# Performance work log

Hardware: AMD Instinct MI355X
Metric: run time of the kernel (lower is better)

Reference implementation:

```python
import jax, jax.numpy as jnp
import numpy as np


def _cross_head_proj(x, sw, qw1, qw2, kw1, kw2, qdd, kdd):
    # x: [B,N,T,S] attention logits/probs; sw: [N,N]
    # qw1/qw2: [B,T,I,N], kw1/kw2: [B,S,I,N] (I=2 dynamic rank), qdd: [B,T,N], kdd: [B,S,N]
    out = x + jnp.einsum('bnts,nm->bmts', x, sw)
    # low-rank dynamic mixing along query positions (sum over i reproduces the range(2) loop)
    qh = jnp.einsum('bnts,btin->bits', x, qw1)          # [B,I,T,S]
    out = out + jnp.einsum('bits,btin->bnts', qh, qw2)
    # low-rank dynamic mixing along key positions
    kh = jnp.einsum('bnts,bsin->bits', x, kw1)          # [B,I,T,S]
    out = out + jnp.einsum('bits,bsin->bnts', kh, kw2)
    # diagonal (per-head) dynamic terms
    out = out + x * jnp.transpose(qdd, (0, 2, 1))[:, :, :, None]   # [B,N,T,1]
    out = out + x * jnp.transpose(kdd, (0, 2, 1))[:, :, None, :]   # [B,N,1,S]
    return out


def setup_inputs() -> dict:
    key = jax.random.key(0)
    ks = jax.random.split(key, 18)
    B, N, T, S, D, I = 1, 32, 1024, 1024, 128, 2
    scale = 0.05  # dynamic weights come out of tanh/RMSnorm in the original; keep them small
    query = jax.random.normal(ks[0], (B, N, T, D), jnp.float32) * (D ** -0.5)
    k_ = jax.random.normal(ks[1], (B, N, S, D), jnp.float32)
    v_ = jax.random.normal(ks[2], (B, N, S, D), jnp.float32)
    neg = jnp.finfo(jnp.float32).min * 0.5  # matches make_causal_mask
    atten_mask = jnp.where(jnp.arange(S)[None, :] <= jnp.arange(T)[:, None], 0.0, neg).astype(jnp.float32)
    def dws(i0):
        return (
            jax.random.normal(ks[i0 + 0], (N, N), jnp.float32) * scale,
            jax.random.normal(ks[i0 + 1], (B, T, I, N), jnp.float32) * scale,
            jax.random.normal(ks[i0 + 2], (B, T, I, N), jnp.float32) * scale,
            jax.random.normal(ks[i0 + 3], (B, S, I, N), jnp.float32) * scale,
            jax.random.normal(ks[i0 + 4], (B, S, I, N), jnp.float32) * scale,
            jax.random.normal(ks[i0 + 5], (B, T, N), jnp.float32) * scale,
            jax.random.normal(ks[i0 + 6], (B, S, N), jnp.float32) * scale,
        )
    sw_pre, qw1_pre, qw2_pre, kw1_pre, kw2_pre, qdd_pre, kdd_pre = dws(3)
    sw_post, qw1_post, qw2_post, kw1_post, kw2_post, qdd_post, kdd_post = dws(10)
    return {
        'query': query, 'key': k_, 'value': v_, 'atten_mask': atten_mask,
        'sw_pre': sw_pre, 'qw1_pre': qw1_pre, 'qw2_pre': qw2_pre, 'kw1_pre': kw1_pre,
        'kw2_pre': kw2_pre, 'qdd_pre': qdd_pre, 'kdd_pre': kdd_pre,
        'sw_post': sw_post, 'qw1_post': qw1_post, 'qw2_post': qw2_post, 'kw1_post': kw1_post,
        'kw2_post': kw2_post, 'qdd_post': qdd_post, 'kdd_post': kdd_post,
    }


def reference(query, key, value, atten_mask,
              sw_pre, qw1_pre, qw2_pre, kw1_pre, kw2_pre, qdd_pre, kdd_pre,
              sw_post, qw1_post, qw2_post, kw1_post, kw2_post, qdd_post, kdd_post):
    # _atten_context: QK^T -> pre cross-head proj -> mask -> softmax -> post cross-head proj -> AV
    logits = jnp.einsum('bntd,bnsd->bnts', query, key)
    logits = _cross_head_proj(logits, sw_pre, qw1_pre, qw2_pre, kw1_pre, kw2_pre, qdd_pre, kdd_pre)
    logits = logits + atten_mask  # [T,S] broadcasts over [B,N,T,S]
    probs = jax.nn.softmax(logits, axis=-1)
    probs = _cross_head_proj(probs, sw_post, qw1_post, qw2_post, kw1_post, kw2_post, qdd_post, kdd_post)
    return jnp.einsum('bnts,bnsd->bntd', probs, value)
```

## Files before the change

kernel.cpp:

```cpp
#include <hip/hip_runtime.h>
#include <hip/hip_bf16.h>
#include <cstdint>
#include <cstddef>

#define T_DIM 1024
#define S_DIM 1024
#define N_HEADS 32
#define D_HEAD 128

typedef __attribute__((ext_vector_type(8))) short short8;
typedef __attribute__((ext_vector_type(4))) float floatx4;

__device__ inline int pack_bf16(float a, float b) {
    __hip_bfloat162 h = __float22bfloat162_rn(make_float2(a, b));
    int r; __builtin_memcpy(&r, &h, 4); return r;
}
__device__ inline ushort f2b(float x) {
    __hip_bfloat16 h = __float2bfloat16(x);
    ushort u; __builtin_memcpy(&u, &h, 2); return u;
}
__device__ inline float b2f(ushort u) {
    unsigned int v = ((unsigned int)u) << 16;
    float f; __builtin_memcpy(&f, &v, 4); return f;
}

__global__ __launch_bounds__(256) void vt_kernel(const float* __restrict__ V,
                                                 ushort* __restrict__ Vt) {
    const int s0 = blockIdx.x * 64;
    const int n  = blockIdx.y;
    __shared__ float lds[128 * 65];

    const int tid = threadIdx.x;
    const float* Vn = V + ((size_t)n * S_DIM + s0) * D_HEAD;

    #pragma unroll
    for (int it = 0; it < 8; ++it) {
        int idx = tid + it * 256;
        int d4 = idx & 31, s = idx >> 5;
        float4 v = *(const float4*)(Vn + (size_t)s * D_HEAD + d4 * 4);
        lds[(d4 * 4 + 0) * 65 + s] = v.x;
        lds[(d4 * 4 + 1) * 65 + s] = v.y;
        lds[(d4 * 4 + 2) * 65 + s] = v.z;
        lds[(d4 * 4 + 3) * 65 + s] = v.w;
    }
    __syncthreads();

    ushort* Vtn = Vt + (size_t)n * D_HEAD * S_DIM;
    #pragma unroll
    for (int it = 0; it < 4; ++it) {
        int idx = tid + it * 256;
        int sg = idx & 7, d = idx >> 3;
        const float* src = &lds[d * 65 + sg * 8];
        int4 o;
        o.x = pack_bf16(src[0], src[1]);
        o.y = pack_bf16(src[2], src[3]);
        o.z = pack_bf16(src[4], src[5]);
        o.w = pack_bf16(src[6], src[7]);
        *(int4*)&Vtn[(size_t)d * S_DIM + s0 + sg * 8] = o;
    }
}

__global__ __launch_bounds__(256, 2) void qk_mfma(const float* __restrict__ Q,
                                                  const float* __restrict__ K,
                                                  ushort* __restrict__ Lb) {
    const int st = blockIdx.x;
    const int tt = blockIdx.y;
    const int n  = blockIdx.z;
    if (st > tt) return;

    __shared__ int Qt[64 * 64];
    __shared__ int Kt[64 * 64];

    const int tid = threadIdx.x;
    const int wv = tid >> 6, ln = tid & 63;
    const int frow = ln & 15, quad = ln >> 4;

    const float* Qn = Q + ((size_t)n * T_DIM + (size_t)tt * 64) * D_HEAD;
    const float* Kn = K + ((size_t)n * S_DIM + (size_t)st * 64) * D_HEAD;

    #pragma unroll
    for (int rep = 0; rep < 8; ++rep) {
        int idx = tid + rep * 256;
        int row = idx >> 5;
        int c4  = (idx & 31) * 4;
        int p   = c4 >> 1;
        int kb  = p >> 4, w = p & 15;
        int swz = 4 * (row & 3);
        float4 q = *(const float4*)(Qn + (size_t)row * D_HEAD + c4);
        int2 qv; qv.x = pack_bf16(q.x, q.y); qv.y = pack_bf16(q.z, q.w);
        *(int2*)&Qt[row * 64 + kb * 16 + (w ^ swz)] = qv;
        float4 k = *(const float4*)(Kn + (size_t)row * D_HEAD + c4);
        int2 kv; kv.x = pack_bf16(k.x, k.y); kv.y = pack_bf16(k.z, k.w);
        *(int2*)&Kt[row * 64 + kb * 16 + (w ^ swz)] = kv;
    }
    __syncthreads();

    const int swz = 4 * (frow & 3);
    floatx4 acc[4] = {};
    #pragma unroll
    for (int kb = 0; kb < 4; ++kb) {
        const short8 af = *(const short8*)&Qt[(wv * 16 + frow) * 64 + kb * 16 + ((quad * 4) ^ swz)];
        #pragma unroll
        for (int si = 0; si < 4; ++si) {
            const short8 bf = *(const short8*)&Kt[(si * 16 + frow) * 64 + kb * 16 + ((quad * 4) ^ swz)];
            acc[si] = __builtin_amdgcn_mfma_f32_16x16x32_bf16(af, bf, acc[si], 0, 0, 0);
        }
    }
    __syncthreads();

    ushort* Ot = (ushort*)Qt;
    #pragma unroll
    for (int si = 0; si < 4; ++si)
        #pragma unroll
        for (int r = 0; r < 4; ++r)
            Ot[(wv * 16 + quad * 4 + r) * 72 + si * 16 + frow] = f2b(acc[si][r]);
    __syncthreads();

    #pragma unroll
    for (int it = 0; it < 2; ++it) {
        int idx = tid + it * 256;
        int row = idx >> 3, col = idx & 7;
        int4 v = *(const int4*)&Ot[row * 72 + col * 8];
        *(int4*)&Lb[((size_t)n * T_DIM + tt * 64 + row) * S_DIM + st * 64 + col * 8] = v;
    }
}

__global__ __launch_bounds__(256) void mat4_kernel(
        const float* __restrict__ sw_pre,  const float* __restrict__ qw1_pre,
        const float* __restrict__ qw2_pre, const float* __restrict__ qdd_pre,
        const float* __restrict__ kw1_pre, const float* __restrict__ kw2_pre,
        const float* __restrict__ kdd_pre,
        const float* __restrict__ sw_post,  const float* __restrict__ qw1_post,
        const float* __restrict__ qw2_post, const float* __restrict__ qdd_post,
        const float* __restrict__ kw1_post, const float* __restrict__ kw2_post,
        const float* __restrict__ kdd_post,
        ushort* __restrict__ mats) {
    const float *sw, *w1, *w2, *dd;
    float idadd;
    switch (blockIdx.y) {
        case 0:  sw = sw_pre;  w1 = qw1_pre;  w2 = qw2_pre;  dd = qdd_pre;  idadd = 1.0f; break;
        case 1:  sw = nullptr; w1 = kw1_pre;  w2 = kw2_pre;  dd = kdd_pre;  idadd = 0.0f; break;
        case 2:  sw = sw_post; w1 = qw1_post; w2 = qw2_post; dd = qdd_post; idadd = 1.0f; break;
        default: sw = nullptr; w1 = kw1_post; w2 = kw2_post; dd = kdd_post; idadd = 0.0f; break;
    }
    ushort* out = mats + (size_t)blockIdx.y * 1024 * 1024;

    const int t = blockIdx.x;
    const int tid = threadIdx.x;
    const int m = tid >> 3;
    const int n0 = (tid & 7) * 4;

    const float w2m0 = w2[t * 64 + m];
    const float w2m1 = w2[t * 64 + 32 + m];
    const float ddm  = dd[t * 32 + m];

    float v[4];
    #pragma unroll
    for (int j = 0; j < 4; ++j) {
        int n = n0 + j;
        float r = w1[t * 64 + n] * w2m0 + w1[t * 64 + 32 + n] * w2m1;
        if (sw) r += sw[n * 32 + m];
        if (n == m) r += idadd + ddm;
        v[j] = r;
    }
    int p0 = pack_bf16(v[0], v[1]);
    int p1 = pack_bf16(v[2], v[3]);
    int2 st = make_int2(p0, p1);
    *(int2*)&out[(size_t)t * 1024 + m * 32 + n0] = st;
}

__global__ __launch_bounds__(256) void rowstat(const ushort* __restrict__ Lb,
                                               float2* __restrict__ stats) {
    const int wv = threadIdx.x >> 6;
    const int ln = threadIdx.x & 63;
    const int r0 = blockIdx.x * 4 + wv;
    const int t  = r0 & (T_DIM - 1);
    const ushort* row = Lb + (size_t)r0 * S_DIM;

    float v[2][8];
    #pragma unroll
    for (int it = 0; it < 2; ++it) {
        const int i0 = it * 512 + ln * 8;
        #pragma unroll
        for (int j = 0; j < 8; ++j) v[it][j] = -INFINITY;
        if (i0 <= t) {
            uint4 raw = *(const uint4*)&row[i0];
            v[it][0] = b2f((ushort)(raw.x & 0xffff)); v[it][1] = b2f((ushort)(raw.x >> 16));
            v[it][2] = b2f((ushort)(raw.y & 0xffff)); v[it][3] = b2f((ushort)(raw.y >> 16));
            v[it][4] = b2f((ushort)(raw.z & 0xffff)); v[it][5] = b2f((ushort)(raw.z >> 16));
            v[it][6] = b2f((ushort)(raw.w & 0xffff)); v[it][7] = b2f((ushort)(raw.w >> 16));
            #pragma unroll
            for (int j = 0; j < 8; ++j)
                if (i0 + j > t) v[it][j] = -INFINITY;
        }
    }

    float m = -INFINITY;
    #pragma unroll
    for (int it = 0; it < 2; ++it)
        #pragma unroll
        for (int j = 0; j < 8; ++j) m = fmaxf(m, v[it][j]);
    #pragma unroll
    for (int off = 32; off > 0; off >>= 1) m = fmaxf(m, __shfl_xor(m, off));

    float ssum = 0.0f;
    #pragma unroll
    for (int it = 0; it < 2; ++it)
        #pragma unroll
        for (int j = 0; j < 8; ++j)
            ssum += (v[it][j] > -1e37f) ? __expf(v[it][j] - m) : 0.0f;
    #pragma unroll
    for (int off = 32; off > 0; off >>= 1) ssum += __shfl_xor(ssum, off);

    if (ln == 0) stats[r0] = make_float2(m, 1.0f / ssum);
}

template<bool SM>
__global__ __launch_bounds__(256, 2) void proj2t(ushort* __restrict__ Lb,
                                                 const ushort* __restrict__ Cmat,
                                                 const ushort* __restrict__ Kmat,
                                                 const float2* __restrict__ stats) {
    const int s0 = blockIdx.x * 32;
    const int t0 = blockIdx.y * 16;
    if (s0 > t0 + 15) return;

    __shared__ __align__(16) ushort Xs[16 * 1288];
    __shared__ __align__(16) float  Kp[16 * 516];

    const int tid = threadIdx.x;
    const int wv = tid >> 6, ln = tid & 63;
    const int frow = ln & 15, quad = ln >> 4;

    #pragma unroll
    for (int it = 0; it < 8; ++it) {
        int slot = tid + it * 256;
        int c    = slot & 3;
        int row  = slot >> 2;
        int nn   = row >> 4, tl = row & 15;
        uint4 ld = *(const uint4*)(Lb + ((size_t)nn * T_DIM + t0 + tl) * S_DIM + s0 + c * 8);
        ushort u[8];
        u[0] = (ushort)(ld.x & 0xffff);  u[1] = (ushort)(ld.x >> 16);
        u[2] = (ushort)(ld.y & 0xffff);  u[3] = (ushort)(ld.y >> 16);
        u[4] = (ushort)(ld.z & 0xffff);  u[5] = (ushort)(ld.z >> 16);
        u[6] = (ushort)(ld.w & 0xffff);  u[7] = (ushort)(ld.w >> 16);
        if (SM) {
            const float2 ms = stats[nn * T_DIM + t0 + tl];
            const int tG = t0 + tl, sbase = s0 + c * 8;
            #pragma unroll
            for (int j = 0; j < 8; ++j) {
                float x = (sbase + j <= tG) ? __expf(b2f(u[j]) - ms.x) * ms.y : 0.0f;
                u[j] = f2b(x);
            }
        }
        ushort* xp = &Xs[tl * 1288 + (c * 8) * 40 + nn];
        #pragma unroll
        for (int j = 0; j < 8; ++j) xp[j * 40] = u[j];
    }
    __syncthreads();

    #pragma unroll
    for (int mh = 0; mh < 2; ++mh) {
        #pragma unroll
        for (int k = 0; k < 8; ++k) {
            const int sl = wv * 8 + k;
            const short8 af = *(const short8*)(Kmat + (size_t)(s0 + sl) * 1024 + (mh * 16 + frow) * 32 + quad * 8);
            const short8 bf = *(const short8*)&Xs[frow * 1288 + sl * 40 + quad * 8];
            floatx4 z = {0.f, 0.f, 0.f, 0.f};
            floatx4 d = __builtin_amdgcn_mfma_f32_16x16x32_bf16(af, bf, z, 0, 0, 0);
            *(floatx4*)&Kp[frow * 516 + sl * 16 + quad * 4] = d;
        }
        __syncthreads();

        #pragma unroll
        for (int i = 0; i < 4; ++i) {
            const int tl = wv * 4 + i;
            const int tg = t0 + tl;
            const short8 bf = *(const short8*)(Cmat + (size_t)tg * 1024 + (mh * 16 + frow) * 32 + quad * 8);
            #pragma unroll
            for (int st = 0; st < 2; ++st) {
                const short8 af = *(const short8*)&Xs[tl * 1288 + (st * 16 + frow) * 40 + quad * 8];
                floatx4 z = {0.f, 0.f, 0.f, 0.f};
                floatx4 d = __builtin_amdgcn_mfma_f32_16x16x32_bf16(af, bf, z, 0, 0, 0);
                float v[4];
                #pragma unroll
                for (int r = 0; r < 4; ++r) {
                    const int sl = st * 16 + quad * 4 + r;
                    float val = d[r] + Kp[tl * 516 + sl * 16 + frow];
                    v[r] = (s0 + sl > tg) ? 0.0f : val;
                }
                uint2 stv;
                stv.x = (unsigned)pack_bf16(v[0], v[1]);
                stv.y = (unsigned)pack_bf16(v[2], v[3]);
                *(uint2*)&Lb[((size_t)(mh * 16 + frow) * T_DIM + tg) * S_DIM + s0 + st * 16 + quad * 4] = stv;
            }
        }
        __syncthreads();
    }
}

__global__ __launch_bounds__(256, 4) void av3(const ushort* __restrict__ P,
                                              const ushort* __restrict__ Vt,
                                              float* __restrict__ O) {
    const int tid = threadIdx.x;
    const int wv = tid >> 6, ln = tid & 63;
    const int frow = ln & 15, quad = ln >> 4;
    const int n  = blockIdx.x;
    const int tt = 63 - blockIdx.y;
    const int t0 = tt * 16;

    __shared__ ushort red[4][16][136];

    const ushort* Pn  = P  + ((size_t)n * T_DIM + t0) * S_DIM;
    const ushort* Vtn = Vt + (size_t)n * D_HEAD * S_DIM;

    const int nsteps = (t0 + 47) >> 5;
    const int nclean = t0 >> 5;

    floatx4 acc[8] = {};
    for (int sb = wv; sb < nsteps; sb += 4) {
        short8 a = *(const short8*)(Pn + (size_t)frow * S_DIM + sb * 32 + quad * 8);
        if (sb >= nclean) {
            const int tg  = t0 + frow;
            const int sg0 = sb * 32 + quad * 8;
            #pragma unroll
            for (int j = 0; j < 8; ++j)
                if (sg0 + j > tg) a[j] = 0;
        }
        #pragma unroll
        for (int dc = 0; dc < 8; ++dc) {
            const short8 b = *(const short8*)(Vtn + (size_t)(dc * 16 + frow) * S_DIM + sb * 32 + quad * 8);
            acc[dc] = __builtin_amdgcn_mfma_f32_16x16x32_bf16(a, b, acc[dc], 0, 0, 0);
        }
    }

    #pragma unroll
    for (int dc = 0; dc < 8; ++dc)
        #pragma unroll
        for (int r = 0; r < 4; ++r)
            red[wv][quad * 4 + r][dc * 16 + frow] = f2b(acc[dc][r]);
    __syncthreads();

    #pragma unroll
    for (int it = 0; it < 2; ++it) {
        int idx = tid + it * 256;
        int d4 = idx & 31, tr = idx >> 5;
        float4 v;
        v.x = b2f(red[0][tr][d4 * 4 + 0]) + b2f(red[1][tr][d4 * 4 + 0]) + b2f(red[2][tr][d4 * 4 + 0]) + b2f(red[3][tr][d4 * 4 + 0]);
        v.y = b2f(red[0][tr][d4 * 4 + 1]) + b2f(red[1][tr][d4 * 4 + 1]) + b2f(red[2][tr][d4 * 4 + 1]) + b2f(red[3][tr][d4 * 4 + 1]);
        v.z = b2f(red[0][tr][d4 * 4 + 2]) + b2f(red[1][tr][d4 * 4 + 2]) + b2f(red[2][tr][d4 * 4 + 2]) + b2f(red[3][tr][d4 * 4 + 2]);
        v.w = b2f(red[0][tr][d4 * 4 + 3]) + b2f(red[1][tr][d4 * 4 + 3]) + b2f(red[2][tr][d4 * 4 + 3]) + b2f(red[3][tr][d4 * 4 + 3]);
        *(float4*)&O[((size_t)n * T_DIM + t0 + tr) * D_HEAD + d4 * 4] = v;
    }
}

extern "C" void kernel_launch(void* const* d_in, const int* in_sizes, int n_in,
                              void* d_out, int out_size, void* d_ws, size_t ws_size,
                              hipStream_t stream) {
    const float* Q    = (const float*)d_in[0];
    const float* K    = (const float*)d_in[1];
    const float* V    = (const float*)d_in[2];
    const float* sw_pre  = (const float*)d_in[4];
    const float* qw1_pre = (const float*)d_in[5];
    const float* qw2_pre = (const float*)d_in[6];
    const float* kw1_pre = (const float*)d_in[7];
    const float* kw2_pre = (const float*)d_in[8];
    const float* qdd_pre = (const float*)d_in[9];
    const float* kdd_pre = (const float*)d_in[10];
    const float* sw_post  = (const float*)d_in[11];
    const float* qw1_post = (const float*)d_in[12];
    const float* qw2_post = (const float*)d_in[13];
    const float* kw1_post = (const float*)d_in[14];
    const float* kw2_post = (const float*)d_in[15];
    const float* qdd_post = (const float*)d_in[16];
    const float* kdd_post = (const float*)d_in[17];

    ushort* Lb = (ushort*)d_ws;
    ushort* Vt = (ushort*)((char*)d_ws + (size_t)N_HEADS * T_DIM * S_DIM * 2);
    float*  O  = (float*)d_out;

    ushort* mats  = (ushort*)d_out;
    ushort* Cpre  = mats + 0 * 1024 * 1024;
    ushort* Kpre  = mats + 1 * 1024 * 1024;
    ushort* Cpost = mats + 2 * 1024 * 1024;
    ushort* Kpost = mats + 3 * 1024 * 1024;
    float2* stats = (float2*)((char*)d_out + (size_t)8 * 1024 * 1024);

    mat4_kernel<<<dim3(1024, 4), 256, 0, stream>>>(
        sw_pre, qw1_pre, qw2_pre, qdd_pre, kw1_pre, kw2_pre, kdd_pre,
        sw_post, qw1_post, qw2_post, qdd_post, kw1_post, kw2_post, kdd_post, mats);
    vt_kernel<<<dim3(16, 32), 256, 0, stream>>>(V, Vt);

    qk_mfma<<<dim3(16, 16, 32), 256, 0, stream>>>(Q, K, Lb);
    proj2t<false><<<dim3(32, 64), 256, 0, stream>>>(Lb, Cpre, Kpre, nullptr);
    rowstat<<<dim3(8192), 256, 0, stream>>>(Lb, stats);
    proj2t<true><<<dim3(32, 64), 256, 0, stream>>>(Lb, Cpost, Kpost, stats);
    av3<<<dim3(32, 64), 256, 0, stream>>>(Lb, Vt, O);
}
```

Measured before the change: 294.1 us.

## Shrink projection kernel LDS with bf16 partials and swizzled head-packed staging

The cross-head projection kernel now stages the logits tile in LDS with a compact XOR-swizzled layout. Each thread loads 8 heads and writes packed 16-byte vectors instead of scattered 2-byte stores. The key-side partial products are kept in LDS as bf16 instead of fp32. Together these cut shared memory so three blocks per CU can fit instead of two, and they reduce LDS store instructions and bank conflicts. The cost is an extra bf16 rounding of the key-mixing partial sum and higher register use for the 8-wide loads.

```diff
diff --git a/kernel.cpp b/kernel.cpp
--- a/kernel.cpp
+++ b/kernel.cpp
@@ -22,6 +22,10 @@
 __device__ inline float b2f(ushort u) {
     unsigned int v = ((unsigned int)u) << 16;
     float f; __builtin_memcpy(&f, &v, 4); return f;
+}
+__device__ inline uint ext16(const uint4& u, int sp) {
+    const uint* p = (const uint*)&u;
+    return (p[sp >> 1] >> ((sp & 1) * 16)) & 0xffffu;
 }
 
 __global__ __launch_bounds__(256) void vt_kernel(const float* __restrict__ V,
@@ -216,45 +220,56 @@
 }
 
 template<bool SM>
-__global__ __launch_bounds__(256, 2) void proj2t(ushort* __restrict__ Lb,
-                                                 const ushort* __restrict__ Cmat,
-                                                 const ushort* __restrict__ Kmat,
-                                                 const float2* __restrict__ stats) {
+__global__ __launch_bounds__(256, 3) void proj3(ushort* __restrict__ Lb,
+                                                const ushort* __restrict__ Cmat,
+                                                const ushort* __restrict__ Kmat,
+                                                const float2* __restrict__ stats) {
     const int s0 = blockIdx.x * 32;
     const int t0 = blockIdx.y * 16;
     if (s0 > t0 + 15) return;
 
-    __shared__ __align__(16) ushort Xs[16 * 1288];
-    __shared__ __align__(16) float  Kp[16 * 516];
+    __shared__ __align__(16) ushort Xs[16 * 1040];
+    __shared__ __align__(16) ushort Kpb[16 * 648];
 
     const int tid = threadIdx.x;
     const int wv = tid >> 6, ln = tid & 63;
     const int frow = ln & 15, quad = ln >> 4;
 
-    #pragma unroll
-    for (int it = 0; it < 8; ++it) {
-        int slot = tid + it * 256;
-        int c    = slot & 3;
-        int row  = slot >> 2;
-        int nn   = row >> 4, tl = row & 15;
-        uint4 ld = *(const uint4*)(Lb + ((size_t)nn * T_DIM + t0 + tl) * S_DIM + s0 + c * 8);
-        ushort u[8];
-        u[0] = (ushort)(ld.x & 0xffff);  u[1] = (ushort)(ld.x >> 16);
-        u[2] = (ushort)(ld.y & 0xffff);  u[3] = (ushort)(ld.y >> 16);
-        u[4] = (ushort)(ld.z & 0xffff);  u[5] = (ushort)(ld.z >> 16);
-        u[6] = (ushort)(ld.w & 0xffff);  u[7] = (ushort)(ld.w >> 16);
+    {
+        const int sc = tid & 3;
+        const int mc = (tid >> 2) & 3;
+        const int tl = tid >> 4;
+        uint4 U[8];
+        #pragma unroll
+        for (int j = 0; j < 8; ++j) {
+            const int n = mc * 8 + j;
+            U[j] = *(const uint4*)(Lb + ((size_t)n * T_DIM + t0 + tl) * S_DIM + s0 + sc * 8);
+        }
         if (SM) {
-            const float2 ms = stats[nn * T_DIM + t0 + tl];
-            const int tG = t0 + tl, sbase = s0 + c * 8;
+            const int tG = t0 + tl;
             #pragma unroll
             for (int j = 0; j < 8; ++j) {
-                float x = (sbase + j <= tG) ? __expf(b2f(u[j]) - ms.x) * ms.y : 0.0f;
-                u[j] = f2b(x);
+                const float2 ms = stats[(mc * 8 + j) * T_DIM + tG];
+                uint* up = (uint*)&U[j];
+                #pragma unroll
+                for (int w = 0; w < 4; ++w) {
+                    const int sg = s0 + sc * 8 + 2 * w;
+                    float lo = (sg     <= tG) ? __expf(b2f((ushort)(up[w] & 0xffff)) - ms.x) * ms.y : 0.0f;
+                    float hi = (sg + 1 <= tG) ? __expf(b2f((ushort)(up[w] >> 16   )) - ms.x) * ms.y : 0.0f;
+                    up[w] = (unsigned)pack_bf16(lo, hi);
+                }
             }
         }
-        ushort* xp = &Xs[tl * 1288 + (c * 8) * 40 + nn];
-        #pragma unroll
-        for (int j = 0; j < 8; ++j) xp[j * 40] = u[j];
+        #pragma unroll
+        for (int sp = 0; sp < 8; ++sp) {
+            const int s = sc * 8 + sp;
+            uint4 W;
+            W.x = ext16(U[0], sp) | (ext16(U[1], sp) << 16);
+            W.y = ext16(U[2], sp) | (ext16(U[3], sp) << 16);
+            W.z = ext16(U[4], sp) | (ext16(U[5], sp) << 16);
+            W.w = ext16(U[6], sp) | (ext16(U[7], sp) << 16);
+            *(uint4*)&Xs[tl * 1040 + s * 32 + ((mc ^ (s & 3)) << 3)] = W;
+        }
     }
     __syncthreads();
 
@@ -264,10 +279,13 @@
         for (int k = 0; k < 8; ++k) {
             const int sl = wv * 8 + k;
             const short8 af = *(const short8*)(Kmat + (size_t)(s0 + sl) * 1024 + (mh * 16 + frow) * 32 + quad * 8);
-            const short8 bf = *(const short8*)&Xs[frow * 1288 + sl * 40 + quad * 8];
+            const short8 bf = *(const short8*)&Xs[frow * 1040 + sl * 32 + ((quad ^ (sl & 3)) << 3)];
             floatx4 z = {0.f, 0.f, 0.f, 0.f};
             floatx4 d = __builtin_amdgcn_mfma_f32_16x16x32_bf16(af, bf, z, 0, 0, 0);
-            *(floatx4*)&Kp[frow * 516 + sl * 16 + quad * 4] = d;
+            uint2 pk;
+            pk.x = (unsigned)pack_bf16(d[0], d[1]);
+            pk.y = (unsigned)pack_bf16(d[2], d[3]);
+            *(uint2*)&Kpb[frow * 648 + sl * 20 + quad * 4] = pk;
         }
         __syncthreads();
 
@@ -278,14 +296,15 @@
             const short8 bf = *(const short8*)(Cmat + (size_t)tg * 1024 + (mh * 16 + frow) * 32 + quad * 8);
             #pragma unroll
             for (int st = 0; st < 2; ++st) {
-                const short8 af = *(const short8*)&Xs[tl * 1288 + (st * 16 + frow) * 40 + quad * 8];
+                const int sA = st * 16 + frow;
+                const short8 af = *(const short8*)&Xs[tl * 1040 + sA * 32 + ((quad ^ (sA & 3)) << 3)];
                 floatx4 z = {0.f, 0.f, 0.f, 0.f};
                 floatx4 d = __builtin_amdgcn_mfma_f32_16x16x32_bf16(af, bf, z, 0, 0, 0);
                 float v[4];
                 #pragma unroll
                 for (int r = 0; r < 4; ++r) {
                     const int sl = st * 16 + quad * 4 + r;
-                    float val = d[r] + Kp[tl * 516 + sl * 16 + frow];
+                    float val = d[r] + b2f(Kpb[tl * 648 + sl * 20 + frow]);
                     v[r] = (s0 + sl > tg) ? 0.0f : val;
                 }
                 uint2 stv;
@@ -391,8 +410,8 @@
     vt_kernel<<<dim3(16, 32), 256, 0, stream>>>(V, Vt);
 
     qk_mfma<<<dim3(16, 16, 32), 256, 0, stream>>>(Q, K, Lb);
-    proj2t<false><<<dim3(32, 64), 256, 0, stream>>>(Lb, Cpre, Kpre, nullptr);
+    proj3<false><<<dim3(32, 64), 256, 0, stream>>>(Lb, Cpre, Kpre, nullptr);
     rowstat<<<dim3(8192), 256, 0, stream>>>(Lb, stats);
-    proj2t<true><<<dim3(32, 64), 256, 0, stream>>>(Lb, Cpost, Kpost, stats);
+    proj3<true><<<dim3(32, 64), 256, 0, stream>>>(Lb, Cpost, Kpost, stats);
     av3<<<dim3(32, 64), 256, 0, stream>>>(Lb, Vt, O);
 }
```

Result: slower. 303.8 us (+3.3%).
